# Kernel optimization log

Hardware: AMD Instinct MI355X
Metric: run time of the kernel (lower is better)

## Reference

```python
import jax, jax.numpy as jnp
import numpy as np

EPS = 1e-5

def _layer_norm(x, gamma, beta):
    m = jnp.mean(x, axis=-1, keepdims=True)
    v = jnp.mean(jnp.square(x - m), axis=-1, keepdims=True)
    return (x - m) * jax.lax.rsqrt(v + EPS) * gamma + beta

def setup_inputs() -> dict:
    key = jax.random.key(0)
    ks = jax.random.split(key, 6)
    B, D, H = 4096, 1024, 1024
    s = 1.0 / np.sqrt(H)
    return {
        "inputs": jax.random.normal(ks[0], (B, D), jnp.float32),
        "hx": jax.random.normal(ks[1], (B, H), jnp.float32),
        "cx": jax.random.normal(ks[2], (B, H), jnp.float32),
        "w_ih": jax.random.uniform(ks[3], (4 * H, D), jnp.float32, -s, s),
        "w_hh": jax.random.uniform(ks[4], (4 * H, H), jnp.float32, -s, s),
        "b_hh": jax.random.uniform(ks[5], (4 * H,), jnp.float32, -s, s),
        "g_ih": jnp.ones((4 * H,), jnp.float32),
        "beta_ih": jnp.zeros((4 * H,), jnp.float32),
        "g_hh": jnp.ones((4 * H,), jnp.float32),
        "beta_hh": jnp.zeros((4 * H,), jnp.float32),
        "g_ho": jnp.ones((H,), jnp.float32),
        "beta_ho": jnp.zeros((H,), jnp.float32),
    }

def reference(inputs, hx, cx, w_ih, w_hh, b_hh, g_ih, beta_ih, g_hh, beta_hh, g_ho, beta_ho):
    # i2h: [B, 4H] (no input bias used in original forward)
    i2h = inputs @ w_ih.T
    h2h = hx @ w_hh.T + b_hh
    gates = _layer_norm(i2h, g_ih, beta_ih) + _layer_norm(h2h, g_hh, beta_hh)
    i, f, o, g = jnp.split(gates, 4, axis=1)  # torch chunk order: i, f, o, g
    cy = jax.nn.sigmoid(f) * cx + jax.nn.sigmoid(i) * jnp.tanh(g)
    hy = jax.nn.sigmoid(o) * _layer_norm(jnp.tanh(cy), g_ho, beta_ho)
    # Dropout(0.1) is identity in eval / deterministic reference
    return hy, cy
```

## Files before the change

kernel.cpp:

```cpp
#include <hip/hip_runtime.h>
#include <hip/hip_bf16.h>
#include <stdint.h>

typedef __attribute__((ext_vector_type(8))) short bf16x8;
typedef __attribute__((ext_vector_type(4))) float f32x4;

#define LN_EPS 1e-5f

__device__ inline unsigned f2bf(float f) {
    unsigned u = __builtin_bit_cast(unsigned, f);
    u += 0x7fffu + ((u >> 16) & 1u);
    return u >> 16;
}
__device__ inline float bf2f(unsigned u) {
    return __builtin_bit_cast(float, u << 16);
}
__device__ inline float sigf(float x) {
    return 1.0f / (1.0f + __expf(-x));
}
__device__ inline float tanh_fast(float x) {
    return __builtin_fmaf(2.0f, 1.0f / (1.0f + __expf(-2.0f * x)), -1.0f);
}
__device__ inline float wred(float v) {
#pragma unroll
    for (int o = 32; o > 0; o >>= 1) v += __shfl_xor(v, o);
    return v;
}
__device__ inline void gload_lds16(const void* g, void* l) {
    __builtin_amdgcn_global_load_lds(
        (const __attribute__((address_space(1))) void*)g,
        (__attribute__((address_space(3))) void*)l, 16, 0, 0);
}

__global__ __launch_bounds__(256) void cast_all(
    const float4* __restrict__ s0, ushort4* __restrict__ d0, int n0,
    const float4* __restrict__ s1, ushort4* __restrict__ d1, int n1,
    const float4* __restrict__ s2, ushort4* __restrict__ d2, int n2,
    const float4* __restrict__ s3, ushort4* __restrict__ d3, int n3)
{
    int j = blockIdx.x * blockDim.x + threadIdx.x;
    const float4* s; ushort4* d;
    if (j < n0) { s = s0; d = d0; }
    else {
        j -= n0;
        if (j < n1) { s = s1; d = d1; }
        else {
            j -= n1;
            if (j < n2) { s = s2; d = d2; }
            else {
                j -= n2;
                if (j >= n3) return;
                s = s3; d = d3;
            }
        }
    }
    float4 v = s[j];
    ushort4 o;
    o.x = (unsigned short)f2bf(v.x); o.y = (unsigned short)f2bf(v.y);
    o.z = (unsigned short)f2bf(v.z); o.w = (unsigned short)f2bf(v.w);
    d[j] = o;
}

#define GNT 32

__global__ __launch_bounds__(512) void gemm8p(
    const short* __restrict__ Aa, const short* __restrict__ Ba, unsigned short* __restrict__ Ca,
    const short* __restrict__ Ab, const short* __restrict__ Bb, unsigned short* __restrict__ Cb,
    const float* __restrict__ Bias,
    float2* __restrict__ P,
    int N, int K)
{
    __shared__ __attribute__((aligned(16))) short lds[65536];
    short* ldsA = lds;
    short* ldsB = lds + 32768;

    const int gx  = gridDim.x;
    const int gxy = gx * gridDim.y;
    int bid = (blockIdx.z * gridDim.y + blockIdx.y) * gx + blockIdx.x;
    const int cpx = (gxy * gridDim.z) >> 3;
    int swz = (bid & 7) * cpx + (bid >> 3);
    const int z  = swz / gxy;
    const int r2 = swz - z * gxy;
    const int by = r2 / gx;
    const int bx = r2 - by * gx;

    const short* __restrict__ A = z ? Ab : Aa;
    const short* __restrict__ B = z ? Bb : Ba;
    unsigned short* __restrict__ C = z ? Cb : Ca;
    const int brow = by * 256, bcol = bx * 256;

    const int t    = threadIdx.x;
    const int lane = t & 63, w = t >> 6;
    const int wr = w >> 2, wc = w & 3;
    const int lr = lane & 15, kc = lane >> 4;

    const int ci0 = t, ci1 = t + 512;
    const int r0 = ci0 >> 2, l0 = (ci0 & 3) ^ ((r0 >> 1) & 3);
    const int r1 = ci1 >> 2, l1 = (ci1 & 3) ^ ((r1 >> 1) & 3);
    const int gA0 = (brow + r0) * K + l0 * 8;
    const int gA1 = (brow + r1) * K + l1 * 8;
    const int gB0 = (bcol + r0) * K + l0 * 8;
    const int gB1 = (bcol + r1) * K + l1 * 8;
    const int d0 = ci0 * 8, d1 = ci1 * 8;

#define STAGE_A(u) { const int so_ = ((u) & 3) * 8192; \
    gload_lds16(A + gA0 + (u) * 32, ldsA + so_ + d0);  \
    gload_lds16(A + gA1 + (u) * 32, ldsA + so_ + d1); }
#define STAGE_B(u) { const int so_ = ((u) & 3) * 8192; \
    gload_lds16(B + gB0 + (u) * 32, ldsB + so_ + d0);  \
    gload_lds16(B + gB1 + (u) * 32, ldsB + so_ + d1); }

    int offW[8], offX[4];
#pragma unroll
    for (int f = 0; f < 8; ++f) {
        int r = wr * 128 + f * 16 + lr;
        offW[f] = r * 32 + ((kc ^ ((r >> 1) & 3)) * 8);
    }
#pragma unroll
    for (int n = 0; n < 4; ++n) {
        int r = wc * 64 + n * 16 + lr;
        offX[n] = r * 32 + ((kc ^ ((r >> 1) & 3)) * 8);
    }

    f32x4 acc[8][4];
#pragma unroll
    for (int i = 0; i < 8; ++i)
#pragma unroll
        for (int j = 0; j < 4; ++j)
            acc[i][j] = (f32x4){0.f, 0.f, 0.f, 0.f};

    STAGE_A(0); STAGE_B(0); STAGE_A(1); STAGE_B(1); STAGE_A(2);
    asm volatile("s_waitcnt vmcnt(6)" ::: "memory");
    __builtin_amdgcn_s_barrier();

#pragma unroll 4
    for (int T = 0; T < GNT; ++T) {
        const int so = (T & 3) * 8192;
        bf16x8 w0, w1, w2, w3, x0, x1, x2, x3;

        w0 = *(const bf16x8*)&ldsB[so + offW[0]];
        w1 = *(const bf16x8*)&ldsB[so + offW[1]];
        w2 = *(const bf16x8*)&ldsB[so + offW[2]];
        w3 = *(const bf16x8*)&ldsB[so + offW[3]];
        x0 = *(const bf16x8*)&ldsA[so + offX[0]];
        x1 = *(const bf16x8*)&ldsA[so + offX[1]];
        x2 = *(const bf16x8*)&ldsA[so + offX[2]];
        x3 = *(const bf16x8*)&ldsA[so + offX[3]];
        if (T + 2 < GNT) STAGE_B(T + 2);
        __builtin_amdgcn_s_barrier();
        asm volatile("s_waitcnt lgkmcnt(0)" ::: "memory");
        __builtin_amdgcn_sched_barrier(0);
        __builtin_amdgcn_s_setprio(1);
        acc[0][0] = __builtin_amdgcn_mfma_f32_16x16x32_bf16(w0, x0, acc[0][0], 0, 0, 0);
        acc[0][1] = __builtin_amdgcn_mfma_f32_16x16x32_bf16(w0, x1, acc[0][1], 0, 0, 0);
        acc[0][2] = __builtin_amdgcn_mfma_f32_16x16x32_bf16(w0, x2, acc[0][2], 0, 0, 0);
        acc[0][3] = __builtin_amdgcn_mfma_f32_16x16x32_bf16(w0, x3, acc[0][3], 0, 0, 0);
        acc[1][0] = __builtin_amdgcn_mfma_f32_16x16x32_bf16(w1, x0, acc[1][0], 0, 0, 0);
        acc[1][1] = __builtin_amdgcn_mfma_f32_16x16x32_bf16(w1, x1, acc[1][1], 0, 0, 0);
        acc[1][2] = __builtin_amdgcn_mfma_f32_16x16x32_bf16(w1, x2, acc[1][2], 0, 0, 0);
        acc[1][3] = __builtin_amdgcn_mfma_f32_16x16x32_bf16(w1, x3, acc[1][3], 0, 0, 0);
        acc[2][0] = __builtin_amdgcn_mfma_f32_16x16x32_bf16(w2, x0, acc[2][0], 0, 0, 0);
        acc[2][1] = __builtin_amdgcn_mfma_f32_16x16x32_bf16(w2, x1, acc[2][1], 0, 0, 0);
        acc[2][2] = __builtin_amdgcn_mfma_f32_16x16x32_bf16(w2, x2, acc[2][2], 0, 0, 0);
        acc[2][3] = __builtin_amdgcn_mfma_f32_16x16x32_bf16(w2, x3, acc[2][3], 0, 0, 0);
        acc[3][0] = __builtin_amdgcn_mfma_f32_16x16x32_bf16(w3, x0, acc[3][0], 0, 0, 0);
        acc[3][1] = __builtin_amdgcn_mfma_f32_16x16x32_bf16(w3, x1, acc[3][1], 0, 0, 0);
        acc[3][2] = __builtin_amdgcn_mfma_f32_16x16x32_bf16(w3, x2, acc[3][2], 0, 0, 0);
        acc[3][3] = __builtin_amdgcn_mfma_f32_16x16x32_bf16(w3, x3, acc[3][3], 0, 0, 0);
        __builtin_amdgcn_s_setprio(0);
        __builtin_amdgcn_s_barrier();

        w0 = *(const bf16x8*)&ldsB[so + offW[4]];
        w1 = *(const bf16x8*)&ldsB[so + offW[5]];
        w2 = *(const bf16x8*)&ldsB[so + offW[6]];
        w3 = *(const bf16x8*)&ldsB[so + offW[7]];
        if (T + 3 < GNT) STAGE_A(T + 3);
        __builtin_amdgcn_s_barrier();
        asm volatile("s_waitcnt lgkmcnt(0)" ::: "memory");
        __builtin_amdgcn_sched_barrier(0);
        __builtin_amdgcn_s_setprio(1);
        acc[4][0] = __builtin_amdgcn_mfma_f32_16x16x32_bf16(w0, x0, acc[4][0], 0, 0, 0);
        acc[4][1] = __builtin_amdgcn_mfma_f32_16x16x32_bf16(w0, x1, acc[4][1], 0, 0, 0);
        acc[4][2] = __builtin_amdgcn_mfma_f32_16x16x32_bf16(w0, x2, acc[4][2], 0, 0, 0);
        acc[4][3] = __builtin_amdgcn_mfma_f32_16x16x32_bf16(w0, x3, acc[4][3], 0, 0, 0);
        acc[5][0] = __builtin_amdgcn_mfma_f32_16x16x32_bf16(w1, x0, acc[5][0], 0, 0, 0);
        acc[5][1] = __builtin_amdgcn_mfma_f32_16x16x32_bf16(w1, x1, acc[5][1], 0, 0, 0);
        acc[5][2] = __builtin_amdgcn_mfma_f32_16x16x32_bf16(w1, x2, acc[5][2], 0, 0, 0);
        acc[5][3] = __builtin_amdgcn_mfma_f32_16x16x32_bf16(w1, x3, acc[5][3], 0, 0, 0);
        acc[6][0] = __builtin_amdgcn_mfma_f32_16x16x32_bf16(w2, x0, acc[6][0], 0, 0, 0);
        acc[6][1] = __builtin_amdgcn_mfma_f32_16x16x32_bf16(w2, x1, acc[6][1], 0, 0, 0);
        acc[6][2] = __builtin_amdgcn_mfma_f32_16x16x32_bf16(w2, x2, acc[6][2], 0, 0, 0);
        acc[6][3] = __builtin_amdgcn_mfma_f32_16x16x32_bf16(w2, x3, acc[6][3], 0, 0, 0);
        acc[7][0] = __builtin_amdgcn_mfma_f32_16x16x32_bf16(w3, x0, acc[7][0], 0, 0, 0);
        acc[7][1] = __builtin_amdgcn_mfma_f32_16x16x32_bf16(w3, x1, acc[7][1], 0, 0, 0);
        acc[7][2] = __builtin_amdgcn_mfma_f32_16x16x32_bf16(w3, x2, acc[7][2], 0, 0, 0);
        acc[7][3] = __builtin_amdgcn_mfma_f32_16x16x32_bf16(w3, x3, acc[7][3], 0, 0, 0);
        __builtin_amdgcn_s_setprio(0);
        if (T < GNT - 3)      { asm volatile("s_waitcnt vmcnt(6)" ::: "memory"); }
        else if (T == GNT - 3){ asm volatile("s_waitcnt vmcnt(4)" ::: "memory"); }
        else if (T == GNT - 2){ asm volatile("s_waitcnt vmcnt(0)" ::: "memory"); }
        __builtin_amdgcn_s_barrier();
    }

    float4 bias4[8];
#pragma unroll
    for (int f = 0; f < 8; ++f) {
        if (z) bias4[f] = *reinterpret_cast<const float4*>(&Bias[bcol + wr * 128 + f * 16 + kc * 4]);
        else   bias4[f] = (float4){0.f, 0.f, 0.f, 0.f};
    }

    uint2 pk[8][4];
    float s[4] = {0.f, 0.f, 0.f, 0.f}, q[4] = {0.f, 0.f, 0.f, 0.f};
#pragma unroll
    for (int f = 0; f < 8; ++f) {
#pragma unroll
        for (int n = 0; n < 4; ++n) {
            float v0 = acc[f][n][0] + bias4[f].x;
            float v1 = acc[f][n][1] + bias4[f].y;
            float v2 = acc[f][n][2] + bias4[f].z;
            float v3 = acc[f][n][3] + bias4[f].w;
            unsigned u0 = f2bf(v0), u1 = f2bf(v1), u2 = f2bf(v2), u3 = f2bf(v3);
            float e0 = bf2f(u0), e1 = bf2f(u1), e2 = bf2f(u2), e3 = bf2f(u3);
            s[n] += (e0 + e1) + (e2 + e3);
            q[n] += (e0 * e0 + e1 * e1) + (e2 * e2 + e3 * e3);
            pk[f][n].x = u0 | (u1 << 16);
            pk[f][n].y = u2 | (u3 << 16);
        }
    }
#pragma unroll
    for (int n = 0; n < 4; ++n) {
        s[n] += __shfl_xor(s[n], 16); s[n] += __shfl_xor(s[n], 32);
        q[n] += __shfl_xor(q[n], 16); q[n] += __shfl_xor(q[n], 32);
    }

    __syncthreads();
    float2* part = (float2*)lds;
    if (kc == 0) {
#pragma unroll
        for (int n = 0; n < 4; ++n) {
            float2 pr; pr.x = s[n]; pr.y = q[n];
            part[wr * 256 + wc * 64 + n * 16 + lr] = pr;
        }
    }
    __syncthreads();
    if (t < 256) {
        float2 p0 = part[t], p1 = part[256 + t];
        float2 o; o.x = p0.x + p1.x; o.y = p0.y + p1.y;
        P[((size_t)(z * 16 + by) * 256 + t) * 16 + bx] = o;
    }
    __syncthreads();

    uint8_t* cb = (uint8_t*)lds;
    const int rloc0 = wc * 64 + lr;
#pragma unroll
    for (int f = 0; f < 8; ++f) {
        const int colB = wr * 256 + f * 32 + kc * 8;
#pragma unroll
        for (int n = 0; n < 4; ++n) {
            const int r = rloc0 + n * 16;
            *reinterpret_cast<uint2*>(cb + r * 512 + (colB ^ ((r & 7) << 4))) = pk[f][n];
        }
    }
    __syncthreads();
    {
        const int rr = t >> 5;
        const int cB = (t & 31) * 16;
#pragma unroll
        for (int i = 0; i < 16; ++i) {
            const int r = rr + i * 16;
            uint4 v = *reinterpret_cast<const uint4*>(cb + r * 512 + (cB ^ ((r & 7) << 4)));
            *reinterpret_cast<uint4*>((uint8_t*)&C[(size_t)(brow + r) * N + bcol] + cB) = v;
        }
    }
#undef STAGE_A
#undef STAGE_B
}

__global__ __launch_bounds__(256) void ln_lstm(
    const unsigned short* __restrict__ i2h,
    const unsigned short* __restrict__ h2h,
    const float* __restrict__ cx,
    const float2* __restrict__ P,
    const float* __restrict__ g_ih, const float* __restrict__ be_ih,
    const float* __restrict__ g_hh, const float* __restrict__ be_hh,
    const float* __restrict__ g_ho, const float* __restrict__ be_ho,
    float* __restrict__ hy, float* __restrict__ cy, int H, int B)
{
    const int b = blockIdx.x;
    const int t = threadIdx.x;
    const int lane = t & 63;
    const int wave = t >> 6;
    const int H4 = 4 * H;
    const int h0 = t * 4;

    const unsigned short* xi = i2h + (size_t)b * H4;
    const unsigned short* xh = h2h + (size_t)b * H4;

    __shared__ float red[4][2];
    __shared__ float st[4];

    if (wave == 0) {
        const int half = (lane >> 4) & 1;
        float2 v = (float2){0.f, 0.f};
        if (lane < 32) v = P[((size_t)(half * B + b)) * 16 + (lane & 15)];
        v.x += __shfl_xor(v.x, 1); v.y += __shfl_xor(v.y, 1);
        v.x += __shfl_xor(v.x, 2); v.y += __shfl_xor(v.y, 2);
        v.x += __shfl_xor(v.x, 4); v.y += __shfl_xor(v.y, 4);
        v.x += __shfl_xor(v.x, 8); v.y += __shfl_xor(v.y, 8);
        if (lane < 32 && (lane & 15) == 0) {
            const float inv4H = 1.0f / (float)H4;
            float m = v.x * inv4H;
            float r = rsqrtf(v.y * inv4H - m * m + LN_EPS);
            st[half * 2]     = m;
            st[half * 2 + 1] = r;
        }
    }
    __syncthreads();
    const float mI = st[0], rI = st[1], mH = st[2], rH = st[3];

    float gate[4][4];
#pragma unroll
    for (int q = 0; q < 4; ++q) {
        const int j = q * H + h0;
        ushort4 vi = *reinterpret_cast<const ushort4*>(&xi[j]);
        ushort4 vh = *reinterpret_cast<const ushort4*>(&xh[j]);
        float4 gi = *reinterpret_cast<const float4*>(&g_ih[j]);
        float4 bi = *reinterpret_cast<const float4*>(&be_ih[j]);
        float4 gh = *reinterpret_cast<const float4*>(&g_hh[j]);
        float4 bh = *reinterpret_cast<const float4*>(&be_hh[j]);
        gate[q][0] = (bf2f(vi.x) - mI) * rI * gi.x + bi.x + (bf2f(vh.x) - mH) * rH * gh.x + bh.x;
        gate[q][1] = (bf2f(vi.y) - mI) * rI * gi.y + bi.y + (bf2f(vh.y) - mH) * rH * gh.y + bh.y;
        gate[q][2] = (bf2f(vi.z) - mI) * rI * gi.z + bi.z + (bf2f(vh.z) - mH) * rH * gh.z + bh.z;
        gate[q][3] = (bf2f(vi.w) - mI) * rI * gi.w + bi.w + (bf2f(vh.w) - mH) * rH * gh.w + bh.w;
    }

    float4 cxv = *reinterpret_cast<const float4*>(&cx[(size_t)b * H + h0]);
    float cvals[4] = {cxv.x, cxv.y, cxv.z, cxv.w};
    float tv[4], ov[4];
    float s2 = 0.f, q2 = 0.f;
    float4 cyv;
#pragma unroll
    for (int k = 0; k < 4; ++k) {
        float c = sigf(gate[1][k]) * cvals[k] + sigf(gate[0][k]) * tanh_fast(gate[3][k]);
        ((float*)&cyv)[k] = c;
        float tc = tanh_fast(c);
        tv[k] = tc; ov[k] = sigf(gate[2][k]);
        s2 += tc; q2 += tc * tc;
    }
    *reinterpret_cast<float4*>(&cy[(size_t)b * H + h0]) = cyv;

    s2 = wred(s2); q2 = wred(q2);
    if (lane == 0) { red[wave][0] = s2; red[wave][1] = q2; }
    __syncthreads();
    float S2 = red[0][0] + red[1][0] + red[2][0] + red[3][0];
    float Q2 = red[0][1] + red[1][1] + red[2][1] + red[3][1];
    const float invH = 1.0f / (float)H;
    float mt = S2 * invH;
    float rt = rsqrtf(Q2 * invH - mt * mt + LN_EPS);

    float4 go = *reinterpret_cast<const float4*>(&g_ho[h0]);
    float4 bo = *reinterpret_cast<const float4*>(&be_ho[h0]);
    float4 hyv;
    hyv.x = ov[0] * ((tv[0] - mt) * rt * go.x + bo.x);
    hyv.y = ov[1] * ((tv[1] - mt) * rt * go.y + bo.y);
    hyv.z = ov[2] * ((tv[2] - mt) * rt * go.z + bo.z);
    hyv.w = ov[3] * ((tv[3] - mt) * rt * go.w + bo.w);
    *reinterpret_cast<float4*>(&hy[(size_t)b * H + h0]) = hyv;
}

extern "C" void kernel_launch(void* const* d_in, const int* in_sizes, int n_in,
                              void* d_out, int out_size, void* d_ws, size_t ws_size,
                              hipStream_t stream) {
    const float* inputs  = (const float*)d_in[0];
    const float* hx      = (const float*)d_in[1];
    const float* cx      = (const float*)d_in[2];
    const float* w_ih    = (const float*)d_in[3];
    const float* w_hh    = (const float*)d_in[4];
    const float* b_hh    = (const float*)d_in[5];
    const float* g_ih    = (const float*)d_in[6];
    const float* beta_ih = (const float*)d_in[7];
    const float* g_hh    = (const float*)d_in[8];
    const float* beta_hh = (const float*)d_in[9];
    const float* g_ho    = (const float*)d_in[10];
    const float* beta_ho = (const float*)d_in[11];

    const int H  = in_sizes[10];
    const int B  = in_sizes[1] / H;
    const int D  = in_sizes[0] / B;
    const int H4 = 4 * H;

    uint8_t* ws = (uint8_t*)d_ws;
    size_t off = 0;
    short* Abf  = (short*)(ws + off); off += (size_t)B * D * 2;
    short* Hbf  = (short*)(ws + off); off += (size_t)B * H * 2;
    short* Wih  = (short*)(ws + off); off += (size_t)H4 * D * 2;
    short* Whh  = (short*)(ws + off); off += (size_t)H4 * H * 2;
    unsigned short* i2hb = (unsigned short*)(ws + off); off += (size_t)B * H4 * 2;
    unsigned short* h2hb = (unsigned short*)(ws + off); off += (size_t)B * H4 * 2;
    float2* P   = (float2*)(ws + off); off += (size_t)2 * B * 16 * sizeof(float2);

    float* hy  = (float*)d_out;
    float* cyo = (float*)d_out + (size_t)B * H;

    {
        const int n0 = (B * D) / 4, n1 = (B * H) / 4, n2 = (H4 * D) / 4, n3 = (H4 * H) / 4;
        const int tot = n0 + n1 + n2 + n3;
        cast_all<<<(tot + 255) / 256, 256, 0, stream>>>(
            (const float4*)inputs, (ushort4*)Abf, n0,
            (const float4*)hx,     (ushort4*)Hbf, n1,
            (const float4*)w_ih,   (ushort4*)Wih, n2,
            (const float4*)w_hh,   (ushort4*)Whh, n3);
    }

    {
        dim3 grid(H4 / 256, B / 256, 2);
        gemm8p<<<grid, 512, 0, stream>>>(Abf, Wih, i2hb, Hbf, Whh, h2hb, b_hh, P, H4, D);
    }

    ln_lstm<<<B, 256, 0, stream>>>(i2hb, h2hb, cx, P,
                                   g_ih, beta_ih, g_hh, beta_hh, g_ho, beta_ho,
                                   hy, cyo, H, B);
}
```

Baseline: 126.5 us.

## Replace 256x256 GEMM tile with 128x128 double-buffered tile kernel

Replaces the 256x256, 512-thread GEMM with a 4-stage LDS ring and split ping-pong phases by a simpler 128x128, 256-thread kernel that double-buffers LDS and targets 4 blocks per CU. The epilogue now writes bf16 results directly from registers instead of staging through LDS for coalesced 16-byte stores. Layer-norm partial sums double to 32 per row, and the LN kernel reduction is adjusted to match. The aim is higher occupancy and simpler scheduling, at the cost of less data reuse per tile, more global traffic, and narrower uncoalesced output stores.

```diff
diff --git a/kernel.cpp b/kernel.cpp
--- a/kernel.cpp
+++ b/kernel.cpp
@@ -61,18 +61,18 @@
     d[j] = o;
 }
 
-#define GNT 32
-
-__global__ __launch_bounds__(512) void gemm8p(
+#define NT 32
+
+__global__ __launch_bounds__(256, 4) void gemm128(
     const short* __restrict__ Aa, const short* __restrict__ Ba, unsigned short* __restrict__ Ca,
     const short* __restrict__ Ab, const short* __restrict__ Bb, unsigned short* __restrict__ Cb,
     const float* __restrict__ Bias,
     float2* __restrict__ P,
-    int N, int K)
+    int N, int K, int Bn)
 {
-    __shared__ __attribute__((aligned(16))) short lds[65536];
+    __shared__ __attribute__((aligned(16))) short lds[16384];
     short* ldsA = lds;
-    short* ldsB = lds + 32768;
+    short* ldsB = lds + 8192;
 
     const int gx  = gridDim.x;
     const int gxy = gx * gridDim.y;
@@ -87,14 +87,14 @@
     const short* __restrict__ A = z ? Ab : Aa;
     const short* __restrict__ B = z ? Bb : Ba;
     unsigned short* __restrict__ C = z ? Cb : Ca;
-    const int brow = by * 256, bcol = bx * 256;
+    const int brow = by * 128, bcol = bx * 128;
 
     const int t    = threadIdx.x;
     const int lane = t & 63, w = t >> 6;
-    const int wr = w >> 2, wc = w & 3;
+    const int wR = w >> 1, wC = w & 1;
     const int lr = lane & 15, kc = lane >> 4;
 
-    const int ci0 = t, ci1 = t + 512;
+    const int ci0 = t, ci1 = t + 256;
     const int r0 = ci0 >> 2, l0 = (ci0 & 3) ^ ((r0 >> 1) & 3);
     const int r1 = ci1 >> 2, l1 = (ci1 & 3) ^ ((r1 >> 1) & 3);
     const int gA0 = (brow + r0) * K + l0 * 8;
@@ -103,54 +103,47 @@
     const int gB1 = (bcol + r1) * K + l1 * 8;
     const int d0 = ci0 * 8, d1 = ci1 * 8;
 
-#define STAGE_A(u) { const int so_ = ((u) & 3) * 8192; \
-    gload_lds16(A + gA0 + (u) * 32, ldsA + so_ + d0);  \
-    gload_lds16(A + gA1 + (u) * 32, ldsA + so_ + d1); }
-#define STAGE_B(u) { const int so_ = ((u) & 3) * 8192; \
-    gload_lds16(B + gB0 + (u) * 32, ldsB + so_ + d0);  \
-    gload_lds16(B + gB1 + (u) * 32, ldsB + so_ + d1); }
-
-    int offW[8], offX[4];
-#pragma unroll
-    for (int f = 0; f < 8; ++f) {
-        int r = wr * 128 + f * 16 + lr;
+#define STG(u, s_) { short* da_ = ldsA + (s_) * 4096; short* db_ = ldsB + (s_) * 4096; \
+    gload_lds16(A + gA0 + (u) * 32, da_ + d0); gload_lds16(A + gA1 + (u) * 32, da_ + d1); \
+    gload_lds16(B + gB0 + (u) * 32, db_ + d0); gload_lds16(B + gB1 + (u) * 32, db_ + d1); }
+
+    int offW[4], offX[4];
+#pragma unroll
+    for (int f = 0; f < 4; ++f) {
+        int r = wC * 64 + f * 16 + lr;
         offW[f] = r * 32 + ((kc ^ ((r >> 1) & 3)) * 8);
     }
 #pragma unroll
     for (int n = 0; n < 4; ++n) {
-        int r = wc * 64 + n * 16 + lr;
+        int r = wR * 64 + n * 16 + lr;
         offX[n] = r * 32 + ((kc ^ ((r >> 1) & 3)) * 8);
     }
 
-    f32x4 acc[8][4];
-#pragma unroll
-    for (int i = 0; i < 8; ++i)
+    f32x4 acc[4][4];
+#pragma unroll
+    for (int i = 0; i < 4; ++i)
 #pragma unroll
         for (int j = 0; j < 4; ++j)
             acc[i][j] = (f32x4){0.f, 0.f, 0.f, 0.f};
 
-    STAGE_A(0); STAGE_B(0); STAGE_A(1); STAGE_B(1); STAGE_A(2);
-    asm volatile("s_waitcnt vmcnt(6)" ::: "memory");
-    __builtin_amdgcn_s_barrier();
-
-#pragma unroll 4
-    for (int T = 0; T < GNT; ++T) {
-        const int so = (T & 3) * 8192;
-        bf16x8 w0, w1, w2, w3, x0, x1, x2, x3;
-
-        w0 = *(const bf16x8*)&ldsB[so + offW[0]];
-        w1 = *(const bf16x8*)&ldsB[so + offW[1]];
-        w2 = *(const bf16x8*)&ldsB[so + offW[2]];
-        w3 = *(const bf16x8*)&ldsB[so + offW[3]];
-        x0 = *(const bf16x8*)&ldsA[so + offX[0]];
-        x1 = *(const bf16x8*)&ldsA[so + offX[1]];
-        x2 = *(const bf16x8*)&ldsA[so + offX[2]];
-        x3 = *(const bf16x8*)&ldsA[so + offX[3]];
-        if (T + 2 < GNT) STAGE_B(T + 2);
-        __builtin_amdgcn_s_barrier();
-        asm volatile("s_waitcnt lgkmcnt(0)" ::: "memory");
-        __builtin_amdgcn_sched_barrier(0);
-        __builtin_amdgcn_s_setprio(1);
+    STG(0, 0);
+    asm volatile("s_waitcnt vmcnt(0)" ::: "memory");
+    __syncthreads();
+
+#pragma unroll 2
+    for (int kt = 0; kt < NT; ++kt) {
+        const int cur = kt & 1;
+        if (kt + 1 < NT) STG(kt + 1, cur ^ 1);
+        const short* bA = ldsA + cur * 4096;
+        const short* bB = ldsB + cur * 4096;
+        bf16x8 w0 = *(const bf16x8*)&bB[offW[0]];
+        bf16x8 w1 = *(const bf16x8*)&bB[offW[1]];
+        bf16x8 w2 = *(const bf16x8*)&bB[offW[2]];
+        bf16x8 w3 = *(const bf16x8*)&bB[offW[3]];
+        bf16x8 x0 = *(const bf16x8*)&bA[offX[0]];
+        bf16x8 x1 = *(const bf16x8*)&bA[offX[1]];
+        bf16x8 x2 = *(const bf16x8*)&bA[offX[2]];
+        bf16x8 x3 = *(const bf16x8*)&bA[offX[3]];
         acc[0][0] = __builtin_amdgcn_mfma_f32_16x16x32_bf16(w0, x0, acc[0][0], 0, 0, 0);
         acc[0][1] = __builtin_amdgcn_mfma_f32_16x16x32_bf16(w0, x1, acc[0][1], 0, 0, 0);
         acc[0][2] = __builtin_amdgcn_mfma_f32_16x16x32_bf16(w0, x2, acc[0][2], 0, 0, 0);
@@ -167,52 +160,22 @@
         acc[3][1] = __builtin_amdgcn_mfma_f32_16x16x32_bf16(w3, x1, acc[3][1], 0, 0, 0);
         acc[3][2] = __builtin_amdgcn_mfma_f32_16x16x32_bf16(w3, x2, acc[3][2], 0, 0, 0);
         acc[3][3] = __builtin_amdgcn_mfma_f32_16x16x32_bf16(w3, x3, acc[3][3], 0, 0, 0);
-        __builtin_amdgcn_s_setprio(0);
-        __builtin_amdgcn_s_barrier();
-
-        w0 = *(const bf16x8*)&ldsB[so + offW[4]];
-        w1 = *(const bf16x8*)&ldsB[so + offW[5]];
-        w2 = *(const bf16x8*)&ldsB[so + offW[6]];
-        w3 = *(const bf16x8*)&ldsB[so + offW[7]];
-        if (T + 3 < GNT) STAGE_A(T + 3);
-        __builtin_amdgcn_s_barrier();
-        asm volatile("s_waitcnt lgkmcnt(0)" ::: "memory");
-        __builtin_amdgcn_sched_barrier(0);
-        __builtin_amdgcn_s_setprio(1);
-        acc[4][0] = __builtin_amdgcn_mfma_f32_16x16x32_bf16(w0, x0, acc[4][0], 0, 0, 0);
-        acc[4][1] = __builtin_amdgcn_mfma_f32_16x16x32_bf16(w0, x1, acc[4][1], 0, 0, 0);
-        acc[4][2] = __builtin_amdgcn_mfma_f32_16x16x32_bf16(w0, x2, acc[4][2], 0, 0, 0);
-        acc[4][3] = __builtin_amdgcn_mfma_f32_16x16x32_bf16(w0, x3, acc[4][3], 0, 0, 0);
-        acc[5][0] = __builtin_amdgcn_mfma_f32_16x16x32_bf16(w1, x0, acc[5][0], 0, 0, 0);
-        acc[5][1] = __builtin_amdgcn_mfma_f32_16x16x32_bf16(w1, x1, acc[5][1], 0, 0, 0);
-        acc[5][2] = __builtin_amdgcn_mfma_f32_16x16x32_bf16(w1, x2, acc[5][2], 0, 0, 0);
-        acc[5][3] = __builtin_amdgcn_mfma_f32_16x16x32_bf16(w1, x3, acc[5][3], 0, 0, 0);
-        acc[6][0] = __builtin_amdgcn_mfma_f32_16x16x32_bf16(w2, x0, acc[6][0], 0, 0, 0);
-        acc[6][1] = __builtin_amdgcn_mfma_f32_16x16x32_bf16(w2, x1, acc[6][1], 0, 0, 0);
-        acc[6][2] = __builtin_amdgcn_mfma_f32_16x16x32_bf16(w2, x2, acc[6][2], 0, 0, 0);
-        acc[6][3] = __builtin_amdgcn_mfma_f32_16x16x32_bf16(w2, x3, acc[6][3], 0, 0, 0);
-        acc[7][0] = __builtin_amdgcn_mfma_f32_16x16x32_bf16(w3, x0, acc[7][0], 0, 0, 0);
-        acc[7][1] = __builtin_amdgcn_mfma_f32_16x16x32_bf16(w3, x1, acc[7][1], 0, 0, 0);
-        acc[7][2] = __builtin_amdgcn_mfma_f32_16x16x32_bf16(w3, x2, acc[7][2], 0, 0, 0);
-        acc[7][3] = __builtin_amdgcn_mfma_f32_16x16x32_bf16(w3, x3, acc[7][3], 0, 0, 0);
-        __builtin_amdgcn_s_setprio(0);
-        if (T < GNT - 3)      { asm volatile("s_waitcnt vmcnt(6)" ::: "memory"); }
-        else if (T == GNT - 3){ asm volatile("s_waitcnt vmcnt(4)" ::: "memory"); }
-        else if (T == GNT - 2){ asm volatile("s_waitcnt vmcnt(0)" ::: "memory"); }
-        __builtin_amdgcn_s_barrier();
-    }
-
-    float4 bias4[8];
-#pragma unroll
-    for (int f = 0; f < 8; ++f) {
-        if (z) bias4[f] = *reinterpret_cast<const float4*>(&Bias[bcol + wr * 128 + f * 16 + kc * 4]);
+        __syncthreads();
+    }
+
+    const int gc0 = bcol + wC * 64 + kc * 4;
+    const int mr0 = brow + wR * 64 + lr;
+
+    float4 bias4[4];
+#pragma unroll
+    for (int f = 0; f < 4; ++f) {
+        if (z) bias4[f] = *reinterpret_cast<const float4*>(&Bias[gc0 + f * 16]);
         else   bias4[f] = (float4){0.f, 0.f, 0.f, 0.f};
     }
 
-    uint2 pk[8][4];
     float s[4] = {0.f, 0.f, 0.f, 0.f}, q[4] = {0.f, 0.f, 0.f, 0.f};
 #pragma unroll
-    for (int f = 0; f < 8; ++f) {
+    for (int f = 0; f < 4; ++f) {
 #pragma unroll
         for (int n = 0; n < 4; ++n) {
             float v0 = acc[f][n][0] + bias4[f].x;
@@ -223,8 +186,8 @@
             float e0 = bf2f(u0), e1 = bf2f(u1), e2 = bf2f(u2), e3 = bf2f(u3);
             s[n] += (e0 + e1) + (e2 + e3);
             q[n] += (e0 * e0 + e1 * e1) + (e2 * e2 + e3 * e3);
-            pk[f][n].x = u0 | (u1 << 16);
-            pk[f][n].y = u2 | (u3 << 16);
+            uint2 pk; pk.x = u0 | (u1 << 16); pk.y = u2 | (u3 << 16);
+            *reinterpret_cast<uint2*>(&C[(size_t)(mr0 + n * 16) * N + gc0 + f * 16]) = pk;
         }
     }
 #pragma unroll
@@ -239,41 +202,16 @@
 #pragma unroll
         for (int n = 0; n < 4; ++n) {
             float2 pr; pr.x = s[n]; pr.y = q[n];
-            part[wr * 256 + wc * 64 + n * 16 + lr] = pr;
+            part[wC * 128 + wR * 64 + n * 16 + lr] = pr;
         }
     }
     __syncthreads();
-    if (t < 256) {
-        float2 p0 = part[t], p1 = part[256 + t];
+    if (t < 128) {
+        float2 p0 = part[t], p1 = part[128 + t];
         float2 o; o.x = p0.x + p1.x; o.y = p0.y + p1.y;
-        P[((size_t)(z * 16 + by) * 256 + t) * 16 + bx] = o;
-    }
-    __syncthreads();
-
-    uint8_t* cb = (uint8_t*)lds;
-    const int rloc0 = wc * 64 + lr;
-#pragma unroll
-    for (int f = 0; f < 8; ++f) {
-        const int colB = wr * 256 + f * 32 + kc * 8;
-#pragma unroll
-        for (int n = 0; n < 4; ++n) {
-            const int r = rloc0 + n * 16;
-            *reinterpret_cast<uint2*>(cb + r * 512 + (colB ^ ((r & 7) << 4))) = pk[f][n];
-        }
-    }
-    __syncthreads();
-    {
-        const int rr = t >> 5;
-        const int cB = (t & 31) * 16;
-#pragma unroll
-        for (int i = 0; i < 16; ++i) {
-            const int r = rr + i * 16;
-            uint4 v = *reinterpret_cast<const uint4*>(cb + r * 512 + (cB ^ ((r & 7) << 4)));
-            *reinterpret_cast<uint4*>((uint8_t*)&C[(size_t)(brow + r) * N + bcol] + cB) = v;
-        }
-    }
-#undef STAGE_A
-#undef STAGE_B
+        P[(size_t)(z * Bn + brow + t) * 32 + bx] = o;
+    }
+#undef STG
 }
 
 __global__ __launch_bounds__(256) void ln_lstm(
@@ -300,14 +238,14 @@
     __shared__ float st[4];
 
     if (wave == 0) {
-        const int half = (lane >> 4) & 1;
-        float2 v = (float2){0.f, 0.f};
-        if (lane < 32) v = P[((size_t)(half * B + b)) * 16 + (lane & 15)];
-        v.x += __shfl_xor(v.x, 1); v.y += __shfl_xor(v.y, 1);
-        v.x += __shfl_xor(v.x, 2); v.y += __shfl_xor(v.y, 2);
-        v.x += __shfl_xor(v.x, 4); v.y += __shfl_xor(v.y, 4);
-        v.x += __shfl_xor(v.x, 8); v.y += __shfl_xor(v.y, 8);
-        if (lane < 32 && (lane & 15) == 0) {
+        const int half = lane >> 5;
+        float2 v = P[((size_t)half * B + b) * 32 + (lane & 31)];
+        v.x += __shfl_xor(v.x, 1);  v.y += __shfl_xor(v.y, 1);
+        v.x += __shfl_xor(v.x, 2);  v.y += __shfl_xor(v.y, 2);
+        v.x += __shfl_xor(v.x, 4);  v.y += __shfl_xor(v.y, 4);
+        v.x += __shfl_xor(v.x, 8);  v.y += __shfl_xor(v.y, 8);
+        v.x += __shfl_xor(v.x, 16); v.y += __shfl_xor(v.y, 16);
+        if ((lane & 31) == 0) {
             const float inv4H = 1.0f / (float)H4;
             float m = v.x * inv4H;
             float r = rsqrtf(v.y * inv4H - m * m + LN_EPS);
@@ -397,7 +335,7 @@
     short* Whh  = (short*)(ws + off); off += (size_t)H4 * H * 2;
     unsigned short* i2hb = (unsigned short*)(ws + off); off += (size_t)B * H4 * 2;
     unsigned short* h2hb = (unsigned short*)(ws + off); off += (size_t)B * H4 * 2;
-    float2* P   = (float2*)(ws + off); off += (size_t)2 * B * 16 * sizeof(float2);
+    float2* P   = (float2*)(ws + off); off += (size_t)2 * B * 32 * sizeof(float2);
 
     float* hy  = (float*)d_out;
     float* cyo = (float*)d_out + (size_t)B * H;
@@ -413,8 +351,8 @@
     }
 
     {
-        dim3 grid(H4 / 256, B / 256, 2);
-        gemm8p<<<grid, 512, 0, stream>>>(Abf, Wih, i2hb, Hbf, Whh, h2hb, b_hh, P, H4, D);
+        dim3 grid(H4 / 128, B / 128, 2);
+        gemm128<<<grid, 256, 0, stream>>>(Abf, Wih, i2hb, Hbf, Whh, h2hb, b_hh, P, H4, D, B);
     }
 
     ln_lstm<<<B, 256, 0, stream>>>(i2hb, h2hb, cx, P,
```

Result: slower. 141.9 us (+12.2%).

## Make each GEMM block compute both i2h and h2h tiles, prefetching the second

Applied to the files above, without the earlier changes.

The launch goes from two z-slices (512 blocks) to 256 blocks that loop over both GEMMs. Loads for the second GEMM are issued before the first GEMM's epilogue so they overlap it. The epilogue drops the LDS-staged coalesced store and writes bf16 results straight from registers. Per-wave partial LN sums go straight to a wider P buffer with no block reduction. Fewer blocks means less tail and launch cost, but uncoalesced 8-byte stores and halved parallelism may hurt.

```diff
diff --git a/kernel.cpp b/kernel.cpp
--- a/kernel.cpp
+++ b/kernel.cpp
@@ -68,25 +68,19 @@
     const short* __restrict__ Ab, const short* __restrict__ Bb, unsigned short* __restrict__ Cb,
     const float* __restrict__ Bias,
     float2* __restrict__ P,
-    int N, int K)
+    int N, int K, int Bn)
 {
-    __shared__ __attribute__((aligned(16))) short lds[65536];
+    __shared__ __attribute__((aligned(16))) short lds[66048];
     short* ldsA = lds;
     short* ldsB = lds + 32768;
-
-    const int gx  = gridDim.x;
-    const int gxy = gx * gridDim.y;
-    int bid = (blockIdx.z * gridDim.y + blockIdx.y) * gx + blockIdx.x;
-    const int cpx = (gxy * gridDim.z) >> 3;
+    float* biasLds = (float*)(lds + 65536);
+
+    const int gx = gridDim.x;
+    int bid = blockIdx.y * gx + blockIdx.x;
+    const int cpx = (gx * gridDim.y) >> 3;
     int swz = (bid & 7) * cpx + (bid >> 3);
-    const int z  = swz / gxy;
-    const int r2 = swz - z * gxy;
-    const int by = r2 / gx;
-    const int bx = r2 - by * gx;
-
-    const short* __restrict__ A = z ? Ab : Aa;
-    const short* __restrict__ B = z ? Bb : Ba;
-    unsigned short* __restrict__ C = z ? Cb : Ca;
+    const int by = swz / gx;
+    const int bx = swz - by * gx;
     const int brow = by * 256, bcol = bx * 256;
 
     const int t    = threadIdx.x;
@@ -103,12 +97,12 @@
     const int gB1 = (bcol + r1) * K + l1 * 8;
     const int d0 = ci0 * 8, d1 = ci1 * 8;
 
-#define STAGE_A(u) { const int so_ = ((u) & 3) * 8192; \
-    gload_lds16(A + gA0 + (u) * 32, ldsA + so_ + d0);  \
-    gload_lds16(A + gA1 + (u) * 32, ldsA + so_ + d1); }
-#define STAGE_B(u) { const int so_ = ((u) & 3) * 8192; \
-    gload_lds16(B + gB0 + (u) * 32, ldsB + so_ + d0);  \
-    gload_lds16(B + gB1 + (u) * 32, ldsB + so_ + d1); }
+#define STAGE_A(PA, u) { const int so_ = ((u) & 3) * 8192; \
+    gload_lds16((PA) + gA0 + (u) * 32, ldsA + so_ + d0);   \
+    gload_lds16((PA) + gA1 + (u) * 32, ldsA + so_ + d1); }
+#define STAGE_B(PB, u) { const int so_ = ((u) & 3) * 8192; \
+    gload_lds16((PB) + gB0 + (u) * 32, ldsB + so_ + d0);   \
+    gload_lds16((PB) + gB1 + (u) * 32, ldsB + so_ + d1); }
 
     int offW[8], offX[4];
 #pragma unroll
@@ -122,154 +116,137 @@
         offX[n] = r * 32 + ((kc ^ ((r >> 1) & 3)) * 8);
     }
 
-    f32x4 acc[8][4];
-#pragma unroll
-    for (int i = 0; i < 8; ++i)
-#pragma unroll
-        for (int j = 0; j < 4; ++j)
-            acc[i][j] = (f32x4){0.f, 0.f, 0.f, 0.f};
-
-    STAGE_A(0); STAGE_B(0); STAGE_A(1); STAGE_B(1); STAGE_A(2);
+    if (t < 64) gload_lds16(Bias + bcol + t * 4, biasLds + t * 4);
+
+    STAGE_A(Aa, 0); STAGE_B(Ba, 0); STAGE_A(Aa, 1); STAGE_B(Ba, 1); STAGE_A(Aa, 2);
     asm volatile("s_waitcnt vmcnt(6)" ::: "memory");
     __builtin_amdgcn_s_barrier();
 
+    for (int zz = 0; zz < 2; ++zz) {
+        const short* A = zz ? Ab : Aa;
+        const short* B = zz ? Bb : Ba;
+        unsigned short* C = zz ? Cb : Ca;
+
+        f32x4 acc[8][4];
+#pragma unroll
+        for (int i = 0; i < 8; ++i)
+#pragma unroll
+            for (int j = 0; j < 4; ++j)
+                acc[i][j] = (f32x4){0.f, 0.f, 0.f, 0.f};
+
 #pragma unroll 4
-    for (int T = 0; T < GNT; ++T) {
-        const int so = (T & 3) * 8192;
-        bf16x8 w0, w1, w2, w3, x0, x1, x2, x3;
-
-        w0 = *(const bf16x8*)&ldsB[so + offW[0]];
-        w1 = *(const bf16x8*)&ldsB[so + offW[1]];
-        w2 = *(const bf16x8*)&ldsB[so + offW[2]];
-        w3 = *(const bf16x8*)&ldsB[so + offW[3]];
-        x0 = *(const bf16x8*)&ldsA[so + offX[0]];
-        x1 = *(const bf16x8*)&ldsA[so + offX[1]];
-        x2 = *(const bf16x8*)&ldsA[so + offX[2]];
-        x3 = *(const bf16x8*)&ldsA[so + offX[3]];
-        if (T + 2 < GNT) STAGE_B(T + 2);
-        __builtin_amdgcn_s_barrier();
-        asm volatile("s_waitcnt lgkmcnt(0)" ::: "memory");
-        __builtin_amdgcn_sched_barrier(0);
-        __builtin_amdgcn_s_setprio(1);
-        acc[0][0] = __builtin_amdgcn_mfma_f32_16x16x32_bf16(w0, x0, acc[0][0], 0, 0, 0);
-        acc[0][1] = __builtin_amdgcn_mfma_f32_16x16x32_bf16(w0, x1, acc[0][1], 0, 0, 0);
-        acc[0][2] = __builtin_amdgcn_mfma_f32_16x16x32_bf16(w0, x2, acc[0][2], 0, 0, 0);
-        acc[0][3] = __builtin_amdgcn_mfma_f32_16x16x32_bf16(w0, x3, acc[0][3], 0, 0, 0);
-        acc[1][0] = __builtin_amdgcn_mfma_f32_16x16x32_bf16(w1, x0, acc[1][0], 0, 0, 0);
-        acc[1][1] = __builtin_amdgcn_mfma_f32_16x16x32_bf16(w1, x1, acc[1][1], 0, 0, 0);
-        acc[1][2] = __builtin_amdgcn_mfma_f32_16x16x32_bf16(w1, x2, acc[1][2], 0, 0, 0);
-        acc[1][3] = __builtin_amdgcn_mfma_f32_16x16x32_bf16(w1, x3, acc[1][3], 0, 0, 0);
-        acc[2][0] = __builtin_amdgcn_mfma_f32_16x16x32_bf16(w2, x0, acc[2][0], 0, 0, 0);
-        acc[2][1] = __builtin_amdgcn_mfma_f32_16x16x32_bf16(w2, x1, acc[2][1], 0, 0, 0);
-        acc[2][2] = __builtin_amdgcn_mfma_f32_16x16x32_bf16(w2, x2, acc[2][2], 0, 0, 0);
-        acc[2][3] = __builtin_amdgcn_mfma_f32_16x16x32_bf16(w2, x3, acc[2][3], 0, 0, 0);
-        acc[3][0] = __builtin_amdgcn_mfma_f32_16x16x32_bf16(w3, x0, acc[3][0], 0, 0, 0);
-        acc[3][1] = __builtin_amdgcn_mfma_f32_16x16x32_bf16(w3, x1, acc[3][1], 0, 0, 0);
-        acc[3][2] = __builtin_amdgcn_mfma_f32_16x16x32_bf16(w3, x2, acc[3][2], 0, 0, 0);
-        acc[3][3] = __builtin_amdgcn_mfma_f32_16x16x32_bf16(w3, x3, acc[3][3], 0, 0, 0);
-        __builtin_amdgcn_s_setprio(0);
-        __builtin_amdgcn_s_barrier();
-
-        w0 = *(const bf16x8*)&ldsB[so + offW[4]];
-        w1 = *(const bf16x8*)&ldsB[so + offW[5]];
-        w2 = *(const bf16x8*)&ldsB[so + offW[6]];
-        w3 = *(const bf16x8*)&ldsB[so + offW[7]];
-        if (T + 3 < GNT) STAGE_A(T + 3);
-        __builtin_amdgcn_s_barrier();
-        asm volatile("s_waitcnt lgkmcnt(0)" ::: "memory");
-        __builtin_amdgcn_sched_barrier(0);
-        __builtin_amdgcn_s_setprio(1);
-        acc[4][0] = __builtin_amdgcn_mfma_f32_16x16x32_bf16(w0, x0, acc[4][0], 0, 0, 0);
-        acc[4][1] = __builtin_amdgcn_mfma_f32_16x16x32_bf16(w0, x1, acc[4][1], 0, 0, 0);
-        acc[4][2] = __builtin_amdgcn_mfma_f32_16x16x32_bf16(w0, x2, acc[4][2], 0, 0, 0);
-        acc[4][3] = __builtin_amdgcn_mfma_f32_16x16x32_bf16(w0, x3, acc[4][3], 0, 0, 0);
-        acc[5][0] = __builtin_amdgcn_mfma_f32_16x16x32_bf16(w1, x0, acc[5][0], 0, 0, 0);
-        acc[5][1] = __builtin_amdgcn_mfma_f32_16x16x32_bf16(w1, x1, acc[5][1], 0, 0, 0);
-        acc[5][2] = __builtin_amdgcn_mfma_f32_16x16x32_bf16(w1, x2, acc[5][2], 0, 0, 0);
-        acc[5][3] = __builtin_amdgcn_mfma_f32_16x16x32_bf16(w1, x3, acc[5][3], 0, 0, 0);
-        acc[6][0] = __builtin_amdgcn_mfma_f32_16x16x32_bf16(w2, x0, acc[6][0], 0, 0, 0);
-        acc[6][1] = __builtin_amdgcn_mfma_f32_16x16x32_bf16(w2, x1, acc[6][1], 0, 0, 0);
-        acc[6][2] = __builtin_amdgcn_mfma_f32_16x16x32_bf16(w2, x2, acc[6][2], 0, 0, 0);
-        acc[6][3] = __builtin_amdgcn_mfma_f32_16x16x32_bf16(w2, x3, acc[6][3], 0, 0, 0);
-        acc[7][0] = __builtin_amdgcn_mfma_f32_16x16x32_bf16(w3, x0, acc[7][0], 0, 0, 0);
-        acc[7][1] = __builtin_amdgcn_mfma_f32_16x16x32_bf16(w3, x1, acc[7][1], 0, 0, 0);
-        acc[7][2] = __builtin_amdgcn_mfma_f32_16x16x32_bf16(w3, x2, acc[7][2], 0, 0, 0);
-        acc[7][3] = __builtin_amdgcn_mfma_f32_16x16x32_bf16(w3, x3, acc[7][3], 0, 0, 0);
-        __builtin_amdgcn_s_setprio(0);
-        if (T < GNT - 3)      { asm volatile("s_waitcnt vmcnt(6)" ::: "memory"); }
-        else if (T == GNT - 3){ asm volatile("s_waitcnt vmcnt(4)" ::: "memory"); }
-        else if (T == GNT - 2){ asm volatile("s_waitcnt vmcnt(0)" ::: "memory"); }
-        __builtin_amdgcn_s_barrier();
-    }
-
-    float4 bias4[8];
-#pragma unroll
-    for (int f = 0; f < 8; ++f) {
-        if (z) bias4[f] = *reinterpret_cast<const float4*>(&Bias[bcol + wr * 128 + f * 16 + kc * 4]);
-        else   bias4[f] = (float4){0.f, 0.f, 0.f, 0.f};
-    }
-
-    uint2 pk[8][4];
-    float s[4] = {0.f, 0.f, 0.f, 0.f}, q[4] = {0.f, 0.f, 0.f, 0.f};
-#pragma unroll
-    for (int f = 0; f < 8; ++f) {
+        for (int T = 0; T < GNT; ++T) {
+            const int so = (T & 3) * 8192;
+            bf16x8 w0, w1, w2, w3, x0, x1, x2, x3;
+
+            w0 = *(const bf16x8*)&ldsB[so + offW[0]];
+            w1 = *(const bf16x8*)&ldsB[so + offW[1]];
+            w2 = *(const bf16x8*)&ldsB[so + offW[2]];
+            w3 = *(const bf16x8*)&ldsB[so + offW[3]];
+            x0 = *(const bf16x8*)&ldsA[so + offX[0]];
+            x1 = *(const bf16x8*)&ldsA[so + offX[1]];
+            x2 = *(const bf16x8*)&ldsA[so + offX[2]];
+            x3 = *(const bf16x8*)&ldsA[so + offX[3]];
+            if (T + 2 < GNT) STAGE_B(B, T + 2);
+            __builtin_amdgcn_s_barrier();
+            asm volatile("s_waitcnt lgkmcnt(0)" ::: "memory");
+            __builtin_amdgcn_sched_barrier(0);
+            __builtin_amdgcn_s_setprio(1);
+            acc[0][0] = __builtin_amdgcn_mfma_f32_16x16x32_bf16(w0, x0, acc[0][0], 0, 0, 0);
+            acc[0][1] = __builtin_amdgcn_mfma_f32_16x16x32_bf16(w0, x1, acc[0][1], 0, 0, 0);
+            acc[0][2] = __builtin_amdgcn_mfma_f32_16x16x32_bf16(w0, x2, acc[0][2], 0, 0, 0);
+            acc[0][3] = __builtin_amdgcn_mfma_f32_16x16x32_bf16(w0, x3, acc[0][3], 0, 0, 0);
+            acc[1][0] = __builtin_amdgcn_mfma_f32_16x16x32_bf16(w1, x0, acc[1][0], 0, 0, 0);
+            acc[1][1] = __builtin_amdgcn_mfma_f32_16x16x32_bf16(w1, x1, acc[1][1], 0, 0, 0);
+            acc[1][2] = __builtin_amdgcn_mfma_f32_16x16x32_bf16(w1, x2, acc[1][2], 0, 0, 0);
+            acc[1][3] = __builtin_amdgcn_mfma_f32_16x16x32_bf16(w1, x3, acc[1][3], 0, 0, 0);
+            acc[2][0] = __builtin_amdgcn_mfma_f32_16x16x32_bf16(w2, x0, acc[2][0], 0, 0, 0);
+            acc[2][1] = __builtin_amdgcn_mfma_f32_16x16x32_bf16(w2, x1, acc[2][1], 0, 0, 0);
+            acc[2][2] = __builtin_amdgcn_mfma_f32_16x16x32_bf16(w2, x2, acc[2][2], 0, 0, 0);
+            acc[2][3] = __builtin_amdgcn_mfma_f32_16x16x32_bf16(w2, x3, acc[2][3], 0, 0, 0);
+            acc[3][0] = __builtin_amdgcn_mfma_f32_16x16x32_bf16(w3, x0, acc[3][0], 0, 0, 0);
+            acc[3][1] = __builtin_amdgcn_mfma_f32_16x16x32_bf16(w3, x1, acc[3][1], 0, 0, 0);
+            acc[3][2] = __builtin_amdgcn_mfma_f32_16x16x32_bf16(w3, x2, acc[3][2], 0, 0, 0);
+            acc[3][3] = __builtin_amdgcn_mfma_f32_16x16x32_bf16(w3, x3, acc[3][3], 0, 0, 0);
+            __builtin_amdgcn_s_setprio(0);
+            __builtin_amdgcn_s_barrier();
+
+            w0 = *(const bf16x8*)&ldsB[so + offW[4]];
+            w1 = *(const bf16x8*)&ldsB[so + offW[5]];
+            w2 = *(const bf16x8*)&ldsB[so + offW[6]];
+            w3 = *(const bf16x8*)&ldsB[so + offW[7]];
+            if (T + 3 < GNT) STAGE_A(A, T + 3);
+            __builtin_amdgcn_s_barrier();
+            asm volatile("s_waitcnt lgkmcnt(0)" ::: "memory");
+            __builtin_amdgcn_sched_barrier(0);
+            __builtin_amdgcn_s_setprio(1);
+            acc[4][0] = __builtin_amdgcn_mfma_f32_16x16x32_bf16(w0, x0, acc[4][0], 0, 0, 0);
+            acc[4][1] = __builtin_amdgcn_mfma_f32_16x16x32_bf16(w0, x1, acc[4][1], 0, 0, 0);
+            acc[4][2] = __builtin_amdgcn_mfma_f32_16x16x32_bf16(w0, x2, acc[4][2], 0, 0, 0);
+            acc[4][3] = __builtin_amdgcn_mfma_f32_16x16x32_bf16(w0, x3, acc[4][3], 0, 0, 0);
+            acc[5][0] = __builtin_amdgcn_mfma_f32_16x16x32_bf16(w1, x0, acc[5][0], 0, 0, 0);
+            acc[5][1] = __builtin_amdgcn_mfma_f32_16x16x32_bf16(w1, x1, acc[5][1], 0, 0, 0);
+            acc[5][2] = __builtin_amdgcn_mfma_f32_16x16x32_bf16(w1, x2, acc[5][2], 0, 0, 0);
+            acc[5][3] = __builtin_amdgcn_mfma_f32_16x16x32_bf16(w1, x3, acc[5][3], 0, 0, 0);
+            acc[6][0] = __builtin_amdgcn_mfma_f32_16x16x32_bf16(w2, x0, acc[6][0], 0, 0, 0);
+            acc[6][1] = __builtin_amdgcn_mfma_f32_16x16x32_bf16(w2, x1, acc[6][1], 0, 0, 0);
+            acc[6][2] = __builtin_amdgcn_mfma_f32_16x16x32_bf16(w2, x2, acc[6][2], 0, 0, 0);
+            acc[6][3] = __builtin_amdgcn_mfma_f32_16x16x32_bf16(w2, x3, acc[6][3], 0, 0, 0);
+            acc[7][0] = __builtin_amdgcn_mfma_f32_16x16x32_bf16(w3, x0, acc[7][0], 0, 0, 0);
+            acc[7][1] = __builtin_amdgcn_mfma_f32_16x16x32_bf16(w3, x1, acc[7][1], 0, 0, 0);
+            acc[7][2] = __builtin_amdgcn_mfma_f32_16x16x32_bf16(w3, x2, acc[7][2], 0, 0, 0);
+            acc[7][3] = __builtin_amdgcn_mfma_f32_16x16x32_bf16(w3, x3, acc[7][3], 0, 0, 0);
+            __builtin_amdgcn_s_setprio(0);
+            if (T < GNT - 3)      { asm volatile("s_waitcnt vmcnt(6)" ::: "memory"); }
+            else if (T == GNT - 3){ asm volatile("s_waitcnt vmcnt(4)" ::: "memory"); }
+            else if (T == GNT - 2){ asm volatile("s_waitcnt vmcnt(0)" ::: "memory"); }
+            __builtin_amdgcn_s_barrier();
+        }
+
+        if (zz == 0) {
+            STAGE_A(Ab, 0); STAGE_B(Bb, 0); STAGE_A(Ab, 1); STAGE_B(Bb, 1); STAGE_A(Ab, 2);
+        }
+
+        const int gc0 = bcol + wr * 128 + kc * 4;
+        const int mr0 = brow + wc * 64 + lr;
+        const int bl0 = wr * 32 + kc;
+
+        float s[4] = {0.f, 0.f, 0.f, 0.f}, q[4] = {0.f, 0.f, 0.f, 0.f};
+#pragma unroll
+        for (int f = 0; f < 8; ++f) {
+            float4 b4;
+            if (zz) b4 = ((const float4*)biasLds)[bl0 + f * 4];
+            else    b4 = (float4){0.f, 0.f, 0.f, 0.f};
+#pragma unroll
+            for (int n = 0; n < 4; ++n) {
+                float v0 = acc[f][n][0] + b4.x;
+                float v1 = acc[f][n][1] + b4.y;
+                float v2 = acc[f][n][2] + b4.z;
+                float v3 = acc[f][n][3] + b4.w;
+                unsigned u0 = f2bf(v0), u1 = f2bf(v1), u2 = f2bf(v2), u3 = f2bf(v3);
+                float e0 = bf2f(u0), e1 = bf2f(u1), e2 = bf2f(u2), e3 = bf2f(u3);
+                s[n] += (e0 + e1) + (e2 + e3);
+                q[n] += (e0 * e0 + e1 * e1) + (e2 * e2 + e3 * e3);
+                uint2 pk; pk.x = u0 | (u1 << 16); pk.y = u2 | (u3 << 16);
+                *reinterpret_cast<uint2*>(&C[(size_t)(mr0 + n * 16) * N + gc0 + f * 16]) = pk;
+            }
+        }
 #pragma unroll
         for (int n = 0; n < 4; ++n) {
-            float v0 = acc[f][n][0] + bias4[f].x;
-            float v1 = acc[f][n][1] + bias4[f].y;
-            float v2 = acc[f][n][2] + bias4[f].z;
-            float v3 = acc[f][n][3] + bias4[f].w;
-            unsigned u0 = f2bf(v0), u1 = f2bf(v1), u2 = f2bf(v2), u3 = f2bf(v3);
-            float e0 = bf2f(u0), e1 = bf2f(u1), e2 = bf2f(u2), e3 = bf2f(u3);
-            s[n] += (e0 + e1) + (e2 + e3);
-            q[n] += (e0 * e0 + e1 * e1) + (e2 * e2 + e3 * e3);
-            pk[f][n].x = u0 | (u1 << 16);
-            pk[f][n].y = u2 | (u3 << 16);
-        }
-    }
-#pragma unroll
-    for (int n = 0; n < 4; ++n) {
-        s[n] += __shfl_xor(s[n], 16); s[n] += __shfl_xor(s[n], 32);
-        q[n] += __shfl_xor(q[n], 16); q[n] += __shfl_xor(q[n], 32);
-    }
-
-    __syncthreads();
-    float2* part = (float2*)lds;
-    if (kc == 0) {
-#pragma unroll
-        for (int n = 0; n < 4; ++n) {
-            float2 pr; pr.x = s[n]; pr.y = q[n];
-            part[wr * 256 + wc * 64 + n * 16 + lr] = pr;
-        }
-    }
-    __syncthreads();
-    if (t < 256) {
-        float2 p0 = part[t], p1 = part[256 + t];
-        float2 o; o.x = p0.x + p1.x; o.y = p0.y + p1.y;
-        P[((size_t)(z * 16 + by) * 256 + t) * 16 + bx] = o;
-    }
-    __syncthreads();
-
-    uint8_t* cb = (uint8_t*)lds;
-    const int rloc0 = wc * 64 + lr;
-#pragma unroll
-    for (int f = 0; f < 8; ++f) {
-        const int colB = wr * 256 + f * 32 + kc * 8;
-#pragma unroll
-        for (int n = 0; n < 4; ++n) {
-            const int r = rloc0 + n * 16;
-            *reinterpret_cast<uint2*>(cb + r * 512 + (colB ^ ((r & 7) << 4))) = pk[f][n];
-        }
-    }
-    __syncthreads();
-    {
-        const int rr = t >> 5;
-        const int cB = (t & 31) * 16;
-#pragma unroll
-        for (int i = 0; i < 16; ++i) {
-            const int r = rr + i * 16;
-            uint4 v = *reinterpret_cast<const uint4*>(cb + r * 512 + (cB ^ ((r & 7) << 4)));
-            *reinterpret_cast<uint4*>((uint8_t*)&C[(size_t)(brow + r) * N + bcol] + cB) = v;
+            s[n] += __shfl_xor(s[n], 16); s[n] += __shfl_xor(s[n], 32);
+            q[n] += __shfl_xor(q[n], 16); q[n] += __shfl_xor(q[n], 32);
+        }
+        if (kc == 0) {
+#pragma unroll
+            for (int n = 0; n < 4; ++n) {
+                float2 pr; pr.x = s[n]; pr.y = q[n];
+                P[(size_t)(zz * Bn + mr0 + n * 16) * 32 + bx * 2 + wr] = pr;
+            }
+        }
+
+        if (zz == 0) {
+            asm volatile("s_waitcnt vmcnt(0)" ::: "memory");
+            __builtin_amdgcn_s_barrier();
         }
     }
 #undef STAGE_A
@@ -300,14 +277,14 @@
     __shared__ float st[4];
 
     if (wave == 0) {
-        const int half = (lane >> 4) & 1;
-        float2 v = (float2){0.f, 0.f};
-        if (lane < 32) v = P[((size_t)(half * B + b)) * 16 + (lane & 15)];
-        v.x += __shfl_xor(v.x, 1); v.y += __shfl_xor(v.y, 1);
-        v.x += __shfl_xor(v.x, 2); v.y += __shfl_xor(v.y, 2);
-        v.x += __shfl_xor(v.x, 4); v.y += __shfl_xor(v.y, 4);
-        v.x += __shfl_xor(v.x, 8); v.y += __shfl_xor(v.y, 8);
-        if (lane < 32 && (lane & 15) == 0) {
+        const int half = lane >> 5;
+        float2 v = P[((size_t)half * B + b) * 32 + (lane & 31)];
+        v.x += __shfl_xor(v.x, 1);  v.y += __shfl_xor(v.y, 1);
+        v.x += __shfl_xor(v.x, 2);  v.y += __shfl_xor(v.y, 2);
+        v.x += __shfl_xor(v.x, 4);  v.y += __shfl_xor(v.y, 4);
+        v.x += __shfl_xor(v.x, 8);  v.y += __shfl_xor(v.y, 8);
+        v.x += __shfl_xor(v.x, 16); v.y += __shfl_xor(v.y, 16);
+        if ((lane & 31) == 0) {
             const float inv4H = 1.0f / (float)H4;
             float m = v.x * inv4H;
             float r = rsqrtf(v.y * inv4H - m * m + LN_EPS);
@@ -397,7 +374,7 @@
     short* Whh  = (short*)(ws + off); off += (size_t)H4 * H * 2;
     unsigned short* i2hb = (unsigned short*)(ws + off); off += (size_t)B * H4 * 2;
     unsigned short* h2hb = (unsigned short*)(ws + off); off += (size_t)B * H4 * 2;
-    float2* P   = (float2*)(ws + off); off += (size_t)2 * B * 16 * sizeof(float2);
+    float2* P   = (float2*)(ws + off); off += (size_t)2 * B * 32 * sizeof(float2);
 
     float* hy  = (float*)d_out;
     float* cyo = (float*)d_out + (size_t)B * H;
@@ -413,8 +390,8 @@
     }
 
     {
-        dim3 grid(H4 / 256, B / 256, 2);
-        gemm8p<<<grid, 512, 0, stream>>>(Abf, Wih, i2hb, Hbf, Whh, h2hb, b_hh, P, H4, D);
+        dim3 grid(H4 / 256, B / 256, 1);
+        gemm8p<<<grid, 512, 0, stream>>>(Abf, Wih, i2hb, Hbf, Whh, h2hb, b_hh, P, H4, D, B);
     }
 
     ln_lstm<<<B, 256, 0, stream>>>(i2hb, h2hb, cx, P,
```

Result: slower. 134.6 us (+6.4%).
